# Kernel optimization log

Measured on AMD Instinct MI355X. Metric: run time of the kernel, lower is better.

## Reference

```python
import jax, jax.numpy as jnp
import numpy as np

BETA_MEM = 0.9
BETA_INH = 0.6
THRESHOLD = 1.0  # snn.Leaky default


def setup_inputs() -> dict:
    key = jax.random.key(0)
    k1, = jax.random.split(key, 1)
    T, B = 1024, 16384
    spike_seq = (jax.random.uniform(k1, (T, B, 2)) < 0.05).astype(jnp.float32)
    w_exc = jnp.array([[0.7, 1.0]], dtype=jnp.float32)  # fc_exc.weight, [1, 2]
    w_inh = jnp.array(-1.0, dtype=jnp.float32)          # scalar inhibitory weight
    return {"spike_seq": spike_seq, "w_exc": w_exc, "w_inh": w_inh}


@jax.custom_vjp
def spike_fn(x):
    # Heaviside spike with ATan surrogate gradient (snntorch default, alpha=2)
    return (x > 0).astype(x.dtype)

def _spike_fwd(x):
    return spike_fn(x), x

def _spike_bwd(x, g):
    return (g / (1.0 + (jnp.pi * x) ** 2),)

spike_fn.defvjp(_spike_fwd, _spike_bwd)


def reference(spike_seq, w_exc, w_inh):
    T, B, _ = spike_seq.shape
    mem0 = jnp.zeros((B, 1), dtype=spike_seq.dtype)
    inh0 = jnp.zeros((B, 1), dtype=spike_seq.dtype)

    def step(carry, x_t):
        mem, inh = carry
        cur_exc = x_t @ w_exc.T                      # [B, 1]
        fm1 = x_t[:, 0:1]                            # [B, 1]
        inh = BETA_INH * inh + fm1
        cur = cur_exc + w_inh * inh
        # snn.Leaky: reset (subtract) computed from previous mem, detached
        reset = jax.lax.stop_gradient((mem - THRESHOLD > 0).astype(mem.dtype))
        mem = BETA_MEM * mem + cur - reset * THRESHOLD
        spk = spike_fn(mem - THRESHOLD)
        return (mem, inh), (spk, mem)

    _, (spk_rec, mem_rec) = jax.lax.scan(step, (mem0, inh0), spike_seq)
    return spk_rec, mem_rec  # each [T, B, 1]
```

## Files before the change

### kernel.cpp

```cpp
#include <hip/hip_runtime.h>

#define T_LEN  1024
#define B_N    16384
#define CHUNKS 32
#define CLEN   (T_LEN / CHUNKS)
#define D_PF   32

__device__ __forceinline__ void neuron_step(float x0, float x1,
                                            float w0, float w1, float wi,
                                            float& mem, float& inh, float& spk) {
#pragma clang fp contract(off)
  const float cur_exc = x0 * w0 + x1 * w1;
  inh = 0.6f * inh + x0;
  const float cur = cur_exc + wi * inh;
  const float reset = (mem - 1.0f > 0.0f) ? 1.0f : 0.0f;
  mem = 0.9f * mem + cur - reset * 1.0f;
  spk = (mem - 1.0f > 0.0f) ? 1.0f : 0.0f;
}

__global__ __launch_bounds__(64, 1) void FMFM_phase1_carry(
    const float* __restrict__ x, const float* __restrict__ w_exc,
    const float* __restrict__ w_inh, float* __restrict__ carry) {
#pragma clang fp contract(off)
  const int b = blockIdx.x * 64 + threadIdx.x;
  const float w0 = w_exc[0], w1 = w_exc[1], wi = w_inh[0];
  const float2* __restrict__ xp = (const float2*)x;

  float mem = 0.0f, inh = 0.0f;
  float spk;

  float2 buf[D_PF];
#pragma unroll
  for (int u = 0; u < D_PF; ++u) buf[u] = xp[u * B_N + b];

  for (int t0 = 0; t0 < T_LEN - D_PF; t0 += D_PF) {
    const int c = t0 / CLEN;
    carry[c * B_N + b] = mem;
    carry[CHUNKS * B_N + c * B_N + b] = inh;
#pragma unroll
    for (int u = 0; u < D_PF; ++u) {
      const float2 v = buf[u];
      buf[u] = xp[(t0 + u + D_PF) * B_N + b];
      neuron_step(v.x, v.y, w0, w1, wi, mem, inh, spk);
    }
  }
  {
    const int t0 = T_LEN - D_PF;
    const int c = t0 / CLEN;
    carry[c * B_N + b] = mem;
    carry[CHUNKS * B_N + c * B_N + b] = inh;
#pragma unroll
    for (int u = 0; u < D_PF; ++u)
      neuron_step(buf[u].x, buf[u].y, w0, w1, wi, mem, inh, spk);
  }
}

__global__ __launch_bounds__(256) void FMFM_phase2_emit(
    const float* __restrict__ x, const float* __restrict__ w_exc,
    const float* __restrict__ w_inh, const float* __restrict__ carry,
    float* __restrict__ out) {
#pragma clang fp contract(off)
  const int c = blockIdx.x >> 6;
  const int b = ((blockIdx.x & 63) << 8) + threadIdx.x;
  const float w0 = w_exc[0], w1 = w_exc[1], wi = w_inh[0];
  const float2* __restrict__ xp = (const float2*)x;

  float mem = carry[c * B_N + b];
  float inh = carry[CHUNKS * B_N + c * B_N + b];
  const int tbase = c * CLEN;

  float2 buf[CLEN];
#pragma unroll
  for (int u = 0; u < CLEN; ++u) buf[u] = xp[(tbase + u) * B_N + b];

  float* __restrict__ spk_out = out;
  float* __restrict__ mem_out = out + (size_t)T_LEN * B_N;
  float spk;
#pragma unroll
  for (int u = 0; u < CLEN; ++u) {
    const int t = tbase + u;
    neuron_step(buf[u].x, buf[u].y, w0, w1, wi, mem, inh, spk);
    __builtin_nontemporal_store(spk, &spk_out[t * B_N + b]);
    __builtin_nontemporal_store(mem, &mem_out[t * B_N + b]);
  }
}

extern "C" void kernel_launch(void* const* d_in, const int* in_sizes, int n_in,
                              void* d_out, int out_size, void* d_ws, size_t ws_size,
                              hipStream_t stream) {
  const float* x     = (const float*)d_in[0];
  const float* w_exc = (const float*)d_in[1];
  const float* w_inh = (const float*)d_in[2];
  float* out   = (float*)d_out;
  float* carry = (float*)d_ws;

  hipLaunchKernelGGL(FMFM_phase1_carry, dim3(B_N / 64), dim3(64), 0, stream,
                     x, w_exc, w_inh, carry);
  hipLaunchKernelGGL(FMFM_phase2_emit, dim3(CHUNKS * (B_N / 256)), dim3(256), 0,
                     stream, x, w_exc, w_inh, carry, out);
}
```

Measured before the change: 279.4 us.

## Pack binary spike inputs into bitmasks before the serial carry scan

```diff
diff --git a/kernel.cpp b/kernel.cpp
--- a/kernel.cpp
+++ b/kernel.cpp
@@ -4,7 +4,9 @@
 #define B_N    16384
 #define CHUNKS 32
 #define CLEN   (T_LEN / CHUNKS)
-#define D_PF   32
+#define TPW    16
+#define NTC    (T_LEN / TPW)
+#define PF     8
 
 __device__ __forceinline__ void neuron_step(float x0, float x1,
                                             float w0, float w1, float wi,
@@ -18,68 +20,88 @@
   spk = (mem - 1.0f > 0.0f) ? 1.0f : 0.0f;
 }
 
-__global__ __launch_bounds__(64, 1) void FMFM_phase1_carry(
-    const float* __restrict__ x, const float* __restrict__ w_exc,
+__global__ __launch_bounds__(256) void FMFM_pack(
+    const float* __restrict__ x, unsigned* __restrict__ cbits) {
+  const int tid = blockIdx.x * 256 + threadIdx.x;
+  const int b2  = tid & (B_N / 2 - 1);
+  const int tc  = tid >> 13;
+  const float4* __restrict__ xp = (const float4*)x;
+
+  unsigned bits0 = 0, bits1 = 0;
+#pragma unroll
+  for (int u = 0; u < TPW; ++u) {
+    const int t = tc * TPW + u;
+    const float4 v = xp[(size_t)t * (B_N / 2) + b2];
+    bits0 |= ((v.x != 0.0f) ? 1u : 0u) << (2 * u);
+    bits0 |= ((v.y != 0.0f) ? 2u : 0u) << (2 * u);
+    bits1 |= ((v.z != 0.0f) ? 1u : 0u) << (2 * u);
+    bits1 |= ((v.w != 0.0f) ? 2u : 0u) << (2 * u);
+  }
+  uint2 w; w.x = bits0; w.y = bits1;
+  *(uint2*)&cbits[(size_t)tc * B_N + 2 * b2] = w;
+}
+
+__global__ __launch_bounds__(64, 1) void FMFM_scan(
+    const unsigned* __restrict__ cbits, const float* __restrict__ w_exc,
     const float* __restrict__ w_inh, float* __restrict__ carry) {
 #pragma clang fp contract(off)
   const int b = blockIdx.x * 64 + threadIdx.x;
   const float w0 = w_exc[0], w1 = w_exc[1], wi = w_inh[0];
-  const float2* __restrict__ xp = (const float2*)x;
+  float mem = 0.0f, inh = 0.0f, spk;
 
-  float mem = 0.0f, inh = 0.0f;
-  float spk;
+  unsigned buf[PF];
+#pragma unroll
+  for (int i = 0; i < PF; ++i) buf[i] = cbits[i * B_N + b];
 
-  float2 buf[D_PF];
+  for (int tc0 = 0; tc0 < NTC; tc0 += PF) {
 #pragma unroll
-  for (int u = 0; u < D_PF; ++u) buf[u] = xp[u * B_N + b];
-
-  for (int t0 = 0; t0 < T_LEN - D_PF; t0 += D_PF) {
-    const int c = t0 / CLEN;
-    carry[c * B_N + b] = mem;
-    carry[CHUNKS * B_N + c * B_N + b] = inh;
+    for (int i = 0; i < PF; ++i) {
+      const int tc = tc0 + i;
+      if ((tc & 1) == 0) {
+        const int c = tc >> 1;
+        carry[c * B_N + b] = mem;
+        carry[(CHUNKS + c) * B_N + b] = inh;
+      }
+      const unsigned w = buf[i];
+      int nx = tc + PF; if (nx > NTC - 1) nx = NTC - 1;
+      buf[i] = cbits[nx * B_N + b];
 #pragma unroll
-    for (int u = 0; u < D_PF; ++u) {
-      const float2 v = buf[u];
-      buf[u] = xp[(t0 + u + D_PF) * B_N + b];
-      neuron_step(v.x, v.y, w0, w1, wi, mem, inh, spk);
+      for (int u = 0; u < TPW; ++u) {
+        const float x0 = (float)((w >> (2 * u)) & 1u);
+        const float x1 = (float)((w >> (2 * u + 1)) & 1u);
+        neuron_step(x0, x1, w0, w1, wi, mem, inh, spk);
+      }
     }
-  }
-  {
-    const int t0 = T_LEN - D_PF;
-    const int c = t0 / CLEN;
-    carry[c * B_N + b] = mem;
-    carry[CHUNKS * B_N + c * B_N + b] = inh;
-#pragma unroll
-    for (int u = 0; u < D_PF; ++u)
-      neuron_step(buf[u].x, buf[u].y, w0, w1, wi, mem, inh, spk);
   }
 }
 
-__global__ __launch_bounds__(256) void FMFM_phase2_emit(
-    const float* __restrict__ x, const float* __restrict__ w_exc,
+__global__ __launch_bounds__(256) void FMFM_emit(
+    const unsigned* __restrict__ cbits, const float* __restrict__ w_exc,
     const float* __restrict__ w_inh, const float* __restrict__ carry,
     float* __restrict__ out) {
 #pragma clang fp contract(off)
   const int c = blockIdx.x >> 6;
   const int b = ((blockIdx.x & 63) << 8) + threadIdx.x;
   const float w0 = w_exc[0], w1 = w_exc[1], wi = w_inh[0];
-  const float2* __restrict__ xp = (const float2*)x;
 
   float mem = carry[c * B_N + b];
-  float inh = carry[CHUNKS * B_N + c * B_N + b];
-  const int tbase = c * CLEN;
-
-  float2 buf[CLEN];
-#pragma unroll
-  for (int u = 0; u < CLEN; ++u) buf[u] = xp[(tbase + u) * B_N + b];
+  float inh = carry[(CHUNKS + c) * B_N + b];
+  const unsigned wa = cbits[(2 * c) * B_N + b];
+  const unsigned wb = cbits[(2 * c + 1) * B_N + b];
 
   float* __restrict__ spk_out = out;
   float* __restrict__ mem_out = out + (size_t)T_LEN * B_N;
+  const int tbase = c * CLEN;
   float spk;
+
 #pragma unroll
   for (int u = 0; u < CLEN; ++u) {
+    const unsigned w = (u < TPW) ? wa : wb;
+    const int s = u & (TPW - 1);
+    const float x0 = (float)((w >> (2 * s)) & 1u);
+    const float x1 = (float)((w >> (2 * s + 1)) & 1u);
+    neuron_step(x0, x1, w0, w1, wi, mem, inh, spk);
     const int t = tbase + u;
-    neuron_step(buf[u].x, buf[u].y, w0, w1, wi, mem, inh, spk);
     __builtin_nontemporal_store(spk, &spk_out[t * B_N + b]);
     __builtin_nontemporal_store(mem, &mem_out[t * B_N + b]);
   }
@@ -91,11 +113,15 @@
   const float* x     = (const float*)d_in[0];
   const float* w_exc = (const float*)d_in[1];
   const float* w_inh = (const float*)d_in[2];
-  float* out   = (float*)d_out;
-  float* carry = (float*)d_ws;
+  float* out = (float*)d_out;
 
-  hipLaunchKernelGGL(FMFM_phase1_carry, dim3(B_N / 64), dim3(64), 0, stream,
-                     x, w_exc, w_inh, carry);
-  hipLaunchKernelGGL(FMFM_phase2_emit, dim3(CHUNKS * (B_N / 256)), dim3(256), 0,
-                     stream, x, w_exc, w_inh, carry, out);
+  unsigned* cbits = (unsigned*)d_ws;
+  float*    carry = (float*)((char*)d_ws + (size_t)NTC * B_N * 4);
+
+  hipLaunchKernelGGL(FMFM_pack, dim3(NTC * (B_N / 2) / 256), dim3(256), 0,
+                     stream, x, cbits);
+  hipLaunchKernelGGL(FMFM_scan, dim3(B_N / 64), dim3(64), 0, stream,
+                     cbits, w_exc, w_inh, carry);
+  hipLaunchKernelGGL(FMFM_emit, dim3(CHUNKS * (B_N / 256)), dim3(256), 0,
+                     stream, cbits, w_exc, w_inh, carry, out);
 }
```

After: 271.4 us. 2.9% less time.
